# Kernel tuning notes

Measured on AMD Instinct MI355X. Metric: run time of the kernel, lower is better.

The kernel has to match this reference:

```python
import jax, jax.numpy as jnp
import numpy as np

EMBED_DIM = 1024
HEADS = 16
HD = EMBED_DIM // HEADS

def setup_inputs() -> dict:
    key = jax.random.key(0)
    ks = jax.random.split(key, 6)
    s = 1.0 / np.sqrt(EMBED_DIM)
    x = jax.random.normal(ks[0], (4, 2048, EMBED_DIM), dtype=jnp.float32)
    Wq = jax.random.uniform(ks[1], (EMBED_DIM, EMBED_DIM), jnp.float32, -s, s)
    Wk = jax.random.uniform(ks[2], (EMBED_DIM, EMBED_DIM), jnp.float32, -s, s)
    Wv = jax.random.uniform(ks[3], (EMBED_DIM, EMBED_DIM), jnp.float32, -s, s)
    Wo = jax.random.uniform(ks[4], (EMBED_DIM, EMBED_DIM), jnp.float32, -s, s)
    bo = jax.random.uniform(ks[5], (EMBED_DIM,), jnp.float32, -s, s)
    return {"x": x, "Wq": Wq, "Wk": Wk, "Wv": Wv, "Wo": Wo, "bo": bo}

def reference(x, Wq, Wk, Wv, Wo, bo):
    B, S, E = x.shape
    # projections (torch Linear: y = x @ W.T), split into heads -> [B,H,S,hd]
    def proj(W):
        return (x @ W.T).reshape(B, S, HEADS, HD).transpose(0, 2, 1, 3)
    q, k, v = proj(Wq), proj(Wk), proj(Wv)
    energy = jnp.einsum('bhid,bhjd->bhij', q, k) / np.sqrt(HD).astype(np.float32)
    causal = jnp.tril(jnp.ones((S, S), dtype=bool))
    energy = jnp.where(causal, energy, -jnp.inf)
    attn = jax.nn.softmax(energy, axis=-1)  # dropout omitted (eval mode)
    out = jnp.einsum('bhij,bhjd->bhid', attn, v)
    out = out.transpose(0, 2, 1, 3).reshape(B, S, E)
    return out @ Wo.T + bo
```

## Files before the change

### kernel.cpp

```cpp
#include <hip/hip_runtime.h>
#include <math.h>

#define EMB   1024
#define HEADS 16
#define HD    64
#define SEQ   2048
#define BATCH 4
#define MTOT  (BATCH * SEQ)
#define XSZ   ((size_t)MTOT * EMB)
#define WSZ   ((size_t)EMB * EMB)

typedef __attribute__((ext_vector_type(8))) short s16x8;
typedef __attribute__((ext_vector_type(4))) short s16x4;
typedef __attribute__((ext_vector_type(4))) float f32x4;

__device__ __forceinline__ short f2bf(float f) {
    unsigned u = __builtin_bit_cast(unsigned, f);
    u += 0x7fffu + ((u >> 16) & 1u);
    return (short)(u >> 16);
}

__device__ __forceinline__ unsigned pk_bf16(float a, float b) {
#if __has_builtin(__builtin_amdgcn_cvt_pk_bf16_f32)
    typedef __attribute__((ext_vector_type(2))) __bf16 bf16x2;
    return __builtin_bit_cast(unsigned, __builtin_amdgcn_cvt_pk_bf16_f32(a, b));
#else
    return (unsigned)(unsigned short)f2bf(a) |
           ((unsigned)(unsigned short)f2bf(b) << 16);
#endif
}

__device__ __forceinline__ float fexp2(float x) {
#if __has_builtin(__builtin_amdgcn_exp2f)
    return __builtin_amdgcn_exp2f(x);
#else
    return exp2f(x);
#endif
}

__device__ __forceinline__ void async16(const void* g, void* l) {
    __builtin_amdgcn_global_load_lds(
        (const __attribute__((address_space(1))) unsigned*)g,
        (__attribute__((address_space(3))) unsigned*)l, 16, 0, 0);
}

__global__ __launch_bounds__(256)
void cvt_inputs(const float* __restrict__ x,  const float* __restrict__ wq,
                const float* __restrict__ wk, const float* __restrict__ wv,
                const float* __restrict__ wo, short* __restrict__ xb,
                short* __restrict__ wcat)
{
    const size_t e = ((size_t)blockIdx.x * 256 + threadIdx.x) * 8;
    const float* src;
    short* dst;
    float scale = 1.0f;
    if (e < XSZ) {
        src = x + e;
        dst = xb + e;
    } else {
        const size_t r = e - XSZ;
        const int w = (int)(r >> 20);
        const size_t off = r & (WSZ - 1);
        src = (w == 0 ? wq : w == 1 ? wk : w == 2 ? wv : wo) + off;
        dst = wcat + r;
        if (w == 0) scale = 0.125f * 1.44269504f;
    }
    const float4 a = ((const float4*)src)[0];
    const float4 b = ((const float4*)src)[1];
    s16x8 v;
    v[0] = f2bf(a.x * scale); v[1] = f2bf(a.y * scale);
    v[2] = f2bf(a.z * scale); v[3] = f2bf(a.w * scale);
    v[4] = f2bf(b.x * scale); v[5] = f2bf(b.y * scale);
    v[6] = f2bf(b.z * scale); v[7] = f2bf(b.w * scale);
    *(s16x8*)dst = v;
}

#define BAR() __builtin_amdgcn_s_barrier()
#define WAIT_LGKM() do { asm volatile("s_waitcnt lgkmcnt(0)" ::: "memory"); \
                         __builtin_amdgcn_sched_barrier(0); } while (0)
#define WAIT_VM(n) asm volatile("s_waitcnt vmcnt(" #n ")" ::: "memory")

#define RD_A(ldsX, qm) \
    _Pragma("unroll") for (int mi = 0; mi < 4; ++mi) \
    _Pragma("unroll") for (int kk = 0; kk < 2; ++kk) \
        a[mi][kk] = *(const s16x8*)((ldsX) + ((qm)*8 + wm*4 + mi) * 2048 + kk * 1024 + abase);

#define RD_B(ldsX, qn, breg) \
    _Pragma("unroll") for (int ni = 0; ni < 2; ++ni) \
    _Pragma("unroll") for (int kk = 0; kk < 2; ++kk) \
        breg[ni][kk] = *(const s16x8*)((ldsX) + ((qn)*8 + wn*2 + ni) * 2048 + kk * 1024 + abase);

#define MFMA_Q(qm, qn, breg) \
    __builtin_amdgcn_s_setprio(1); \
    _Pragma("unroll") for (int mi = 0; mi < 4; ++mi) \
    _Pragma("unroll") for (int ni = 0; ni < 2; ++ni) \
    _Pragma("unroll") for (int kk = 0; kk < 2; ++kk) \
        acc[(qm)*4+mi][(qn)*2+ni] = __builtin_amdgcn_mfma_f32_16x16x32_bf16( \
            a[mi][kk], breg[ni][kk], acc[(qm)*4+mi][(qn)*2+ni], 0, 0, 0); \
    __builtin_amdgcn_s_setprio(0);

#define STAGE(pM, ldsMat, h, k0) do { \
    async16((pM) + (size_t)((h) * 128) * K + (k0),      (ldsMat) + (h) * 16384 + wv1024); \
    async16((pM) + (size_t)((h) * 128 + 64) * K + (k0), (ldsMat) + (h) * 16384 + 8192 + wv1024); \
} while (0)

template<bool OUT_BF16>
__global__ __launch_bounds__(512, 2)
void gemm_8ph(const short* __restrict__ A, const short* __restrict__ B,
              void* __restrict__ C, int ldc, const float* __restrict__ bias,
              int K)
{
    __shared__ __align__(16) char lds[131072];
    char* ldsA0 = lds;
    char* ldsB0 = lds + 32768;
    char* ldsA1 = lds + 65536;
    char* ldsB1 = lds + 98304;

    const int tid   = threadIdx.x;
    const int wv    = tid >> 6;
    const int lane  = tid & 63;
    const int col16 = lane & 15;
    const int quad  = lane >> 4;
    const int wm    = wv >> 2;
    const int wn    = wv & 3;
    const int wv1024 = wv << 10;

    const int nwg = gridDim.x * gridDim.y;
    int wg = blockIdx.y * gridDim.x + blockIdx.x;
    wg = (wg & 7) * (nwg >> 3) + (wg >> 3);
    const int rowBase = (wg / gridDim.x) * 256;
    const int colBase = (wg % gridDim.x) * 256;

    const int abase = (col16 * 64 + quad * 16) ^ ((col16 & 8) << 2);

    const int rlane = (lane >> 2) & 15;
    const int rw0   = ((wv >> 1) << 4) + rlane;
    const int colSt = ((wv & 1) << 5) + (((lane & 3) << 3) ^ ((lane & 32) >> 1));
    const short* pA = A + (size_t)(rowBase + rw0) * K + colSt;
    const short* pB = B + (size_t)(colBase + rw0) * K + colSt;

    s16x8 a[4][2], bq0[2][2], bq1[2][2];
    f32x4 acc[8][4];
#pragma unroll
    for (int i = 0; i < 8; ++i)
#pragma unroll
        for (int j = 0; j < 4; ++j) acc[i][j] = (f32x4){0.f, 0.f, 0.f, 0.f};

    const int NITER = K >> 7;

    STAGE(pA, ldsA0, 0, 0);
    STAGE(pA, ldsA0, 1, 0);
    STAGE(pB, ldsB0, 0, 0);
    STAGE(pB, ldsB0, 1, 0);
    STAGE(pA, ldsA1, 0, 64);
    STAGE(pB, ldsB1, 0, 64);
    WAIT_VM(4);
    BAR();

    for (int it = 0; it < NITER; ++it) {
        const int k0 = it << 7;
        const bool more = (it + 1 < NITER);

        RD_A(ldsA0, 0); RD_B(ldsB0, 0, bq0);
        STAGE(pA, ldsA1, 1, k0 + 64);
        BAR(); WAIT_LGKM();
        MFMA_Q(0, 0, bq0);
        BAR();
        RD_B(ldsB0, 1, bq1);
        STAGE(pB, ldsB1, 1, k0 + 64);
        BAR(); WAIT_LGKM();
        MFMA_Q(0, 1, bq1);
        BAR();
        RD_A(ldsA0, 1);
        if (more) STAGE(pA, ldsA0, 0, k0 + 128);
        BAR(); WAIT_LGKM();
        MFMA_Q(1, 0, bq0);
        BAR();
        if (more) STAGE(pB, ldsB0, 0, k0 + 128);
        BAR();
        MFMA_Q(1, 1, bq1);
        if (more) { WAIT_VM(4); } else { WAIT_VM(0); }
        BAR();
        RD_A(ldsA1, 0); RD_B(ldsB1, 0, bq0);
        if (more) STAGE(pA, ldsA0, 1, k0 + 128);
        BAR(); WAIT_LGKM();
        MFMA_Q(0, 0, bq0);
        BAR();
        RD_B(ldsB1, 1, bq1);
        if (more) STAGE(pB, ldsB0, 1, k0 + 128);
        BAR(); WAIT_LGKM();
        MFMA_Q(0, 1, bq1);
        BAR();
        RD_A(ldsA1, 1);
        if (more) STAGE(pA, ldsA1, 0, k0 + 192);
        BAR(); WAIT_LGKM();
        MFMA_Q(1, 0, bq0);
        BAR();
        if (more) STAGE(pB, ldsB1, 0, k0 + 192);
        BAR();
        MFMA_Q(1, 1, bq1);
        WAIT_VM(4);
        BAR();
    }

    if (OUT_BF16) {
        short* Cb = (short*)C;
#pragma unroll
        for (int qm = 0; qm < 2; ++qm)
#pragma unroll
        for (int mi = 0; mi < 4; ++mi) {
            const int rg0 = rowBase + qm * 128 + wm * 64 + mi * 16 + quad * 4;
#pragma unroll
            for (int qn = 0; qn < 2; ++qn)
#pragma unroll
            for (int ni = 0; ni < 2; ++ni) {
                const int cg = colBase + qn * 128 + wn * 32 + ni * 16 + col16;
                const f32x4 v = acc[qm * 4 + mi][qn * 2 + ni];
#pragma unroll
                for (int r = 0; r < 4; ++r)
                    Cb[(size_t)(rg0 + r) * ldc + cg] = f2bf(v[r]);
            }
        }
    } else {
        float* Cf = (float*)C;
#pragma unroll
        for (int qn = 0; qn < 2; ++qn)
#pragma unroll
        for (int ni = 0; ni < 2; ++ni) {
            const int cg = colBase + qn * 128 + wn * 32 + ni * 16 + col16;
            const float bj = bias ? bias[cg] : 0.f;
#pragma unroll
            for (int qm = 0; qm < 2; ++qm)
#pragma unroll
            for (int mi = 0; mi < 4; ++mi) {
                const int rg0 = rowBase + qm * 128 + wm * 64 + mi * 16 + quad * 4;
                const f32x4 v = acc[qm * 4 + mi][qn * 2 + ni];
#pragma unroll
                for (int r = 0; r < 4; ++r)
                    Cf[(size_t)(rg0 + r) * ldc + cg] = v[r] + bj;
            }
        }
    }
}

#define LDQ 3072
__global__ __launch_bounds__(512)
void attn_mfma(const short* __restrict__ QKV, short* __restrict__ O)
{
    __shared__ short lK[64 * 72];
    __shared__ short lV[64 * 72];
    __shared__ short lP[8 * 32 * 72];

    const int tid  = threadIdx.x;
    const int wv   = tid >> 6;
    const int lane = tid & 63;
    const int col  = lane & 15;
    const int quad = lane >> 4;

    const int bh = blockIdx.y;
    const int b  = bh >> 4;
    const int h  = bh & 15;
    const size_t baseq = (size_t)b * SEQ * LDQ + (size_t)h * HD;
    const size_t basek = baseq + 1024;
    const size_t basev = baseq + 2048;
    const size_t baseo = (size_t)b * SEQ * EMB + (size_t)h * HD;

    const int krow = tid >> 3;
    const int kc0  = (tid & 7) * 8;
    short* pwave = &lP[(wv * 32) * 72];

    const s16x8 onesv = {0x3F80, 0x3F80, 0x3F80, 0x3F80,
                         0x3F80, 0x3F80, 0x3F80, 0x3F80};

    for (int half = 0; half < 2; ++half) {
        const int qsuper = half ? (7 - (int)blockIdx.x) : (int)blockIdx.x;
        const int qb = qsuper * 256;
        const int qlo_w = qb + wv * 32;

        s16x8 qf[2][2];
#pragma unroll
        for (int rb = 0; rb < 2; ++rb) {
            const short* qr = QKV + baseq + (size_t)(qlo_w + rb * 16 + col) * LDQ;
            qf[rb][0] = *(const s16x8*)(qr + quad * 8);
            qf[rb][1] = *(const s16x8*)(qr + 32 + quad * 8);
        }

        f32x4 of[2][4], lsum[2];
#pragma unroll
        for (int rb = 0; rb < 2; ++rb) {
#pragma unroll
            for (int u = 0; u < 4; ++u) of[rb][u] = (f32x4){0.f, 0.f, 0.f, 0.f};
            lsum[rb] = (f32x4){0.f, 0.f, 0.f, 0.f};
        }

        const int nt = qb / 64 + 4;

        s16x8 pk = *(const s16x8*)(QKV + basek + (size_t)krow * LDQ + kc0);
        s16x8 pv = *(const s16x8*)(QKV + basev + (size_t)lane * LDQ + wv * 8);

        for (int kt = 0; kt < nt; ++kt) {
            const int kb = kt * 64;
            __syncthreads();
            *(s16x8*)&lK[krow * 72 + kc0] = pk;
#pragma unroll
            for (int t = 0; t < 8; ++t)
                lV[(wv * 8 + t) * 72 + lane] = pv[t];
            __syncthreads();

            if (kt + 1 < nt) {
                pk = *(const s16x8*)(QKV + basek + (size_t)(kb + 64 + krow) * LDQ + kc0);
                pv = *(const s16x8*)(QKV + basev + (size_t)(kb + 64 + lane) * LDQ + wv * 8);
            }

            if (kb > qlo_w + 31) continue;

            s16x8 kf[4][2];
#pragma unroll
            for (int t = 0; t < 4; ++t) {
                kf[t][0] = *(const s16x8*)&lK[(t * 16 + col) * 72 + quad * 8];
                kf[t][1] = *(const s16x8*)&lK[(t * 16 + col) * 72 + 32 + quad * 8];
            }

#pragma unroll
            for (int rb = 0; rb < 2; ++rb) {
                const int qlo = qlo_w + rb * 16;
                const int qg  = qlo + col;

                f32x4 s[4];
#pragma unroll
                for (int t = 0; t < 4; ++t) {
                    f32x4 acc = (f32x4){0.f, 0.f, 0.f, 0.f};
                    acc = __builtin_amdgcn_mfma_f32_16x16x32_bf16(kf[t][0], qf[rb][0], acc, 0, 0, 0);
                    acc = __builtin_amdgcn_mfma_f32_16x16x32_bf16(kf[t][1], qf[rb][1], acc, 0, 0, 0);
                    s[t] = acc;
                }

                if (kb + 63 > qlo) {
#pragma unroll
                    for (int t = 0; t < 4; ++t)
#pragma unroll
                        for (int rr = 0; rr < 4; ++rr) {
                            const int kg = kb + t * 16 + quad * 4 + rr;
                            if (kg > qg) s[t][rr] = -3.0e38f;
                        }
                }

                short* pbase = pwave + (rb * 16) * 72;
#pragma unroll
                for (int t = 0; t < 4; ++t) {
                    uint2 pkd;
                    pkd.x = pk_bf16(fexp2(s[t][0]), fexp2(s[t][1]));
                    pkd.y = pk_bf16(fexp2(s[t][2]), fexp2(s[t][3]));
                    *(uint2*)&pbase[col * 72 + t * 16 + quad * 4] = pkd;
                }
            }

#pragma unroll
            for (int c = 0; c < 2; ++c) {
                s16x8 vf[4];
#pragma unroll
                for (int u = 0; u < 4; ++u)
                    vf[u] = *(const s16x8*)&lV[(u * 16 + col) * 72 + c * 32 + quad * 8];
#pragma unroll
                for (int rb = 0; rb < 2; ++rb) {
                    const s16x8 pa = *(const s16x8*)&pwave[(rb * 16 + col) * 72 + c * 32 + quad * 8];
                    lsum[rb] = __builtin_amdgcn_mfma_f32_16x16x32_bf16(onesv, pa, lsum[rb], 0, 0, 0);
#pragma unroll
                    for (int u = 0; u < 4; ++u)
                        of[rb][u] = __builtin_amdgcn_mfma_f32_16x16x32_bf16(vf[u], pa, of[rb][u], 0, 0, 0);
                }
            }
        }

#pragma unroll
        for (int rb = 0; rb < 2; ++rb) {
            const float rl = 1.f / lsum[rb][0];
            short* orow = O + baseo + (size_t)(qlo_w + rb * 16 + col) * EMB + quad * 4;
#pragma unroll
            for (int u = 0; u < 4; ++u) {
                uint2 pkd;
                pkd.x = pk_bf16(of[rb][u][0] * rl, of[rb][u][1] * rl);
                pkd.y = pk_bf16(of[rb][u][2] * rl, of[rb][u][3] * rl);
                *(uint2*)&orow[u * 16] = pkd;
            }
        }
    }
}

extern "C" void kernel_launch(void* const* d_in, const int* in_sizes, int n_in,
                              void* d_out, int out_size, void* d_ws, size_t ws_size,
                              hipStream_t stream)
{
    const float* x  = (const float*)d_in[0];
    const float* Wq = (const float*)d_in[1];
    const float* Wk = (const float*)d_in[2];
    const float* Wv = (const float*)d_in[3];
    const float* Wo = (const float*)d_in[4];
    const float* bo = (const float*)d_in[5];
    float* out = (float*)d_out;

    short* xb   = (short*)d_ws;
    short* wcat = xb + XSZ;
    short* qkv  = wcat + 4 * WSZ;
    short* ob   = qkv + (size_t)MTOT * 3 * EMB;

    const int cvt_blocks = (int)((XSZ + 4 * WSZ) / 8 / 256);
    cvt_inputs<<<cvt_blocks, 256, 0, stream>>>(x, Wq, Wk, Wv, Wo, xb, wcat);

    gemm_8ph<true><<<dim3(3072 / 256, MTOT / 256), 512, 0, stream>>>(
        xb, wcat, qkv, 3072, nullptr, EMB);

    attn_mfma<<<dim3(4, BATCH * HEADS), 512, 0, stream>>>(qkv, ob);

    gemm_8ph<false><<<dim3(EMB / 256, MTOT / 256), 512, 0, stream>>>(
        ob, wcat + (size_t)3 * WSZ, out, EMB, bo, EMB);
}
```

Measured before the change: 251.7 us.

## Replace 8-phase GEMM with 256x128 tiles and triple-buffered 64-wide K pipeline

The projection and output GEMMs move from 256x256 tiles with a double-buffered 128-wide K step to 256x128 tiles with a three-slot ring of 64-wide K stages. Loads for step k+2 are issued while step k computes. Waves now cover a 64x64 sub-tile each instead of splitting into quadrants, and the grid doubles along N. This is meant to deepen memory latency hiding, cut accumulator registers, and add workgroups for better CU fill on the small output GEMM. The cost is lower arithmetic intensity per tile and 144KB of LDS, which may limit occupancy to one block per CU.

```diff
diff --git a/kernel.cpp b/kernel.cpp
--- a/kernel.cpp
+++ b/kernel.cpp
@@ -80,56 +80,59 @@
                          __builtin_amdgcn_sched_barrier(0); } while (0)
 #define WAIT_VM(n) asm volatile("s_waitcnt vmcnt(" #n ")" ::: "memory")
 
-#define RD_A(ldsX, qm) \
+#define RD_A4(bA) \
     _Pragma("unroll") for (int mi = 0; mi < 4; ++mi) \
     _Pragma("unroll") for (int kk = 0; kk < 2; ++kk) \
-        a[mi][kk] = *(const s16x8*)((ldsX) + ((qm)*8 + wm*4 + mi) * 2048 + kk * 1024 + abase);
-
-#define RD_B(ldsX, qn, breg) \
+        a[mi][kk] = *(const s16x8*)((bA) + (wm4 + mi) * 2048 + kk * 1024 + abase);
+
+#define RD_B2(bB, hf, breg) \
     _Pragma("unroll") for (int ni = 0; ni < 2; ++ni) \
     _Pragma("unroll") for (int kk = 0; kk < 2; ++kk) \
-        breg[ni][kk] = *(const s16x8*)((ldsX) + ((qn)*8 + wn*2 + ni) * 2048 + kk * 1024 + abase);
-
-#define MFMA_Q(qm, qn, breg) \
+        breg[ni][kk] = *(const s16x8*)((bB) + (wn4 + (hf) * 2 + ni) * 2048 + kk * 1024 + abase);
+
+#define MFMA16(hf, breg) \
     __builtin_amdgcn_s_setprio(1); \
     _Pragma("unroll") for (int mi = 0; mi < 4; ++mi) \
     _Pragma("unroll") for (int ni = 0; ni < 2; ++ni) \
     _Pragma("unroll") for (int kk = 0; kk < 2; ++kk) \
-        acc[(qm)*4+mi][(qn)*2+ni] = __builtin_amdgcn_mfma_f32_16x16x32_bf16( \
-            a[mi][kk], breg[ni][kk], acc[(qm)*4+mi][(qn)*2+ni], 0, 0, 0); \
+        acc[mi][(hf) * 2 + ni] = __builtin_amdgcn_mfma_f32_16x16x32_bf16( \
+            a[mi][kk], breg[ni][kk], acc[mi][(hf) * 2 + ni], 0, 0, 0); \
     __builtin_amdgcn_s_setprio(0);
 
-#define STAGE(pM, ldsMat, h, k0) do { \
-    async16((pM) + (size_t)((h) * 128) * K + (k0),      (ldsMat) + (h) * 16384 + wv1024); \
-    async16((pM) + (size_t)((h) * 128 + 64) * K + (k0), (ldsMat) + (h) * 16384 + 8192 + wv1024); \
+#define STA(pM, ldsM, h, k0) do { \
+    async16((pM) + (size_t)((h) * 128) * K + (k0),      (ldsM) + (h) * 16384 + wv1024); \
+    async16((pM) + (size_t)((h) * 128 + 64) * K + (k0), (ldsM) + (h) * 16384 + 8192 + wv1024); \
+} while (0)
+
+#define STB(pM, ldsM, k0) do { \
+    async16((pM) + (k0),                (ldsM) + wv1024); \
+    async16((pM) + (size_t)64 * K + (k0), (ldsM) + 8192 + wv1024); \
 } while (0)
 
 template<bool OUT_BF16>
 __global__ __launch_bounds__(512, 2)
-void gemm_8ph(const short* __restrict__ A, const short* __restrict__ B,
-              void* __restrict__ C, int ldc, const float* __restrict__ bias,
-              int K)
+void gemm_qp(const short* __restrict__ A, const short* __restrict__ B,
+             void* __restrict__ C, int ldc, const float* __restrict__ bias,
+             int K)
 {
-    __shared__ __align__(16) char lds[131072];
-    char* ldsA0 = lds;
-    char* ldsB0 = lds + 32768;
-    char* ldsA1 = lds + 65536;
-    char* ldsB1 = lds + 98304;
+    __shared__ __align__(16) char lds[147456];
 
     const int tid   = threadIdx.x;
     const int wv    = tid >> 6;
     const int lane  = tid & 63;
     const int col16 = lane & 15;
     const int quad  = lane >> 4;
-    const int wm    = wv >> 2;
-    const int wn    = wv & 3;
+    const int wm    = wv >> 1;
+    const int wn    = wv & 1;
+    const int wm4   = wm * 4;
+    const int wn4   = wn * 4;
     const int wv1024 = wv << 10;
 
     const int nwg = gridDim.x * gridDim.y;
     int wg = blockIdx.y * gridDim.x + blockIdx.x;
     wg = (wg & 7) * (nwg >> 3) + (wg >> 3);
     const int rowBase = (wg / gridDim.x) * 256;
-    const int colBase = (wg % gridDim.x) * 256;
+    const int colBase = (wg % gridDim.x) * 128;
 
     const int abase = (col16 * 64 + quad * 16) ^ ((col16 & 8) << 2);
 
@@ -140,82 +143,53 @@
     const short* pB = B + (size_t)(colBase + rw0) * K + colSt;
 
     s16x8 a[4][2], bq0[2][2], bq1[2][2];
-    f32x4 acc[8][4];
-#pragma unroll
-    for (int i = 0; i < 8; ++i)
+    f32x4 acc[4][4];
+#pragma unroll
+    for (int i = 0; i < 4; ++i)
 #pragma unroll
         for (int j = 0; j < 4; ++j) acc[i][j] = (f32x4){0.f, 0.f, 0.f, 0.f};
 
-    const int NITER = K >> 7;
-
-    STAGE(pA, ldsA0, 0, 0);
-    STAGE(pA, ldsA0, 1, 0);
-    STAGE(pB, ldsB0, 0, 0);
-    STAGE(pB, ldsB0, 1, 0);
-    STAGE(pA, ldsA1, 0, 64);
-    STAGE(pB, ldsB1, 0, 64);
-    WAIT_VM(4);
+    const int NT = K >> 6;
+
+    char* r0 = lds;
+    char* r1 = lds + 49152;
+    char* r2 = lds + 98304;
+
+    STA(pA, r0, 0, 0);  STA(pA, r0, 1, 0);  STB(pB, r0 + 32768, 0);
+    STA(pA, r1, 0, 64); STA(pA, r1, 1, 64); STB(pB, r1 + 32768, 64);
+    WAIT_VM(6);
     BAR();
 
-    for (int it = 0; it < NITER; ++it) {
-        const int k0 = it << 7;
-        const bool more = (it + 1 < NITER);
-
-        RD_A(ldsA0, 0); RD_B(ldsB0, 0, bq0);
-        STAGE(pA, ldsA1, 1, k0 + 64);
+    for (int kt = 0; kt < NT; ++kt) {
+        const int k0 = kt << 6;
+        const bool more = (kt + 2 < NT);
+
+        RD_A4(r0);
+        RD_B2(r0 + 32768, 0, bq0);
+        if (more) { STA(pA, r2, 0, k0 + 128); STB(pB, r2 + 32768, k0 + 128); }
         BAR(); WAIT_LGKM();
-        MFMA_Q(0, 0, bq0);
+        MFMA16(0, bq0);
         BAR();
-        RD_B(ldsB0, 1, bq1);
-        STAGE(pB, ldsB1, 1, k0 + 64);
+
+        RD_B2(r0 + 32768, 1, bq1);
+        if (more) STA(pA, r2, 1, k0 + 128);
         BAR(); WAIT_LGKM();
-        MFMA_Q(0, 1, bq1);
+        MFMA16(1, bq1);
+        if (more) { WAIT_VM(6); } else { WAIT_VM(0); }
         BAR();
-        RD_A(ldsA0, 1);
-        if (more) STAGE(pA, ldsA0, 0, k0 + 128);
-        BAR(); WAIT_LGKM();
-        MFMA_Q(1, 0, bq0);
-        BAR();
-        if (more) STAGE(pB, ldsB0, 0, k0 + 128);
-        BAR();
-        MFMA_Q(1, 1, bq1);
-        if (more) { WAIT_VM(4); } else { WAIT_VM(0); }
-        BAR();
-        RD_A(ldsA1, 0); RD_B(ldsB1, 0, bq0);
-        if (more) STAGE(pA, ldsA0, 1, k0 + 128);
-        BAR(); WAIT_LGKM();
-        MFMA_Q(0, 0, bq0);
-        BAR();
-        RD_B(ldsB1, 1, bq1);
-        if (more) STAGE(pB, ldsB0, 1, k0 + 128);
-        BAR(); WAIT_LGKM();
-        MFMA_Q(0, 1, bq1);
-        BAR();
-        RD_A(ldsA1, 1);
-        if (more) STAGE(pA, ldsA1, 0, k0 + 192);
-        BAR(); WAIT_LGKM();
-        MFMA_Q(1, 0, bq0);
-        BAR();
-        if (more) STAGE(pB, ldsB1, 0, k0 + 192);
-        BAR();
-        MFMA_Q(1, 1, bq1);
-        WAIT_VM(4);
-        BAR();
+
+        char* t = r0; r0 = r1; r1 = r2; r2 = t;
     }
 
     if (OUT_BF16) {
         short* Cb = (short*)C;
 #pragma unroll
-        for (int qm = 0; qm < 2; ++qm)
-#pragma unroll
         for (int mi = 0; mi < 4; ++mi) {
-            const int rg0 = rowBase + qm * 128 + wm * 64 + mi * 16 + quad * 4;
-#pragma unroll
-            for (int qn = 0; qn < 2; ++qn)
-#pragma unroll
-            for (int ni = 0; ni < 2; ++ni) {
-                const int cg = colBase + qn * 128 + wn * 32 + ni * 16 + col16;
-                const f32x4 v = acc[qm * 4 + mi][qn * 2 + ni];
+            const int rg0 = rowBase + wm * 64 + mi * 16 + quad * 4;
+#pragma unroll
+            for (int ni = 0; ni < 4; ++ni) {
+                const int cg = colBase + wn * 64 + ni * 16 + col16;
+                const f32x4 v = acc[mi][ni];
 #pragma unroll
                 for (int r = 0; r < 4; ++r)
                     Cb[(size_t)(rg0 + r) * ldc + cg] = f2bf(v[r]);
@@ -224,17 +198,13 @@
     } else {
         float* Cf = (float*)C;
 #pragma unroll
-        for (int qn = 0; qn < 2; ++qn)
-#pragma unroll
-        for (int ni = 0; ni < 2; ++ni) {
-            const int cg = colBase + qn * 128 + wn * 32 + ni * 16 + col16;
+        for (int ni = 0; ni < 4; ++ni) {
+            const int cg = colBase + wn * 64 + ni * 16 + col16;
             const float bj = bias ? bias[cg] : 0.f;
 #pragma unroll
-            for (int qm = 0; qm < 2; ++qm)
-#pragma unroll
             for (int mi = 0; mi < 4; ++mi) {
-                const int rg0 = rowBase + qm * 128 + wm * 64 + mi * 16 + quad * 4;
-                const f32x4 v = acc[qm * 4 + mi][qn * 2 + ni];
+                const int rg0 = rowBase + wm * 64 + mi * 16 + quad * 4;
+                const f32x4 v = acc[mi][ni];
 #pragma unroll
                 for (int r = 0; r < 4; ++r)
                     Cf[(size_t)(rg0 + r) * ldc + cg] = v[r] + bj;
@@ -407,11 +377,11 @@
     const int cvt_blocks = (int)((XSZ + 4 * WSZ) / 8 / 256);
     cvt_inputs<<<cvt_blocks, 256, 0, stream>>>(x, Wq, Wk, Wv, Wo, xb, wcat);
 
-    gemm_8ph<true><<<dim3(3072 / 256, MTOT / 256), 512, 0, stream>>>(
+    gemm_qp<true><<<dim3(3072 / 128, MTOT / 256), 512, 0, stream>>>(
         xb, wcat, qkv, 3072, nullptr, EMB);
 
     attn_mfma<<<dim3(4, BATCH * HEADS), 512, 0, stream>>>(qkv, ob);
 
-    gemm_8ph<false><<<dim3(EMB / 256, MTOT / 256), 512, 0, stream>>>(
+    gemm_qp<false><<<dim3(EMB / 128, MTOT / 256), 512, 0, stream>>>(
         ob, wcat + (size_t)3 * WSZ, out, EMB, bo, EMB);
 }
```

Result: faster. 243.9 us (-3.1%).
